# Optimization experiments

Hardware: AMD Instinct MI355X
Metric: run time of the kernel (lower is better)

The kernel has to match this reference:

```python
import jax, jax.numpy as jnp
import numpy as np

SR = 16000
FLOOR = 60.0
EPS = 1e-12

# ---------- numpy helpers replicating the torch control flow (plan building) ----------

def _hann(n):
    # torch.hann_window default periodic=True: 0.5 - 0.5*cos(2*pi*k/n)
    if n <= 0:
        return np.zeros((0,), np.float32)
    return (0.5 - 0.5 * np.cos(2.0 * np.pi * np.arange(n) / n)).astype(np.float32)


def _interp_linear(p, T):
    # torch F.interpolate(mode='linear', align_corners=False) on [1,1,S] -> [1,1,T]
    S = p.shape[0]
    pos = (np.arange(T, dtype=np.float64) + 0.5) * (S / T) - 0.5
    pos = np.clip(pos, 0.0, S - 1)
    lo = np.floor(pos).astype(np.int64)
    hi = np.minimum(lo + 1, S - 1)
    frac = pos - lo
    return (p[lo] * (1.0 - frac) + p[hi] * frac).astype(np.float32)


def _find_voiced(f0, i):
    sub = f0[i:]
    if sub.size == 0:
        return None
    flag = (sub > 0.0).astype(np.int64)
    flag[0] = 0
    if not flag.any():
        return None
    idx = int(flag.argmax())
    rest = flag[idx:]
    z = np.nonzero(rest == 0)[0]
    cnt = int(z[0]) if z.size else int(rest.size)
    left = i + idx
    return left, left + cnt


def _find_allpeaks(sig, f0, sr, floor=FLOOR):
    T = sig.shape[0]
    gpeak = float(np.abs(sig).max())

    def find_peak(i, dir_):
        w = int(sr / max(float(f0[i]), floor))
        s = max(i - w // 2, 0)
        if dir_ == 'left':
            cl, cr = max(int(i - 1.75 * w), 0), max(int(i - 1.3 * w), 0)
        else:
            cl, cr = int(i + 0.3 * w), int(i + 0.75 * w)
        if cl == cr or T - cl < w or s + w > T:
            return w, -1.0, i, 0.0
        seg = np.lib.stride_tricks.sliding_window_view(sig[cl:min(T, cr + w)], w)
        segn = seg / np.maximum(np.linalg.norm(seg, axis=-1, keepdims=True), EPS)
        tmpl = sig[s:s + w]
        tmpl = tmpl / max(float(np.linalg.norm(tmpl)), EPS)
        corr = segn @ tmpl
        r = int(corr.argmax())
        return w, float(corr[r]), i + (r + cl) - s, float(np.abs(seg[r]).max())

    added_right, i, peaks = -1e308, 0, []
    while True:
        v = _find_voiced(f0, i)
        if v is None:
            break
        left, right = v
        middle = (left + right) // 2
        w = int(sr / float(f0[middle]))
        s = max(middle - w // 2, 0)
        win = sig[s:s + w]
        mn, imn = float(win.min()), int(win.argmin())
        mx, imx = float(win.max()), int(win.argmax())
        if mn == mx:
            i = middle
        else:
            i = s + (imn if abs(mn) > abs(mx) else imx)
        backup = i
        while True:
            w, corr, i, peak = find_peak(i, 'left')
            if corr == -1.0:
                i -= w
            if i < left:
                if corr > 0.7 and peak > 0.023333 * gpeak and i - added_right > 0.8 * w:
                    peaks.append(i)
                break
            if corr > 0.3 and (peak == 0.0 or peak > 0.01 * gpeak):
                if i - added_right > 0.8 * w:
                    peaks.append(i)
        i = backup
        while True:
            w, corr, i, peak = find_peak(i, 'right')
            if corr == -1.0:
                i += w
            if i >= right:
                if corr > 0.7 and peak > 0.023333 * gpeak:
                    peaks.append(i)
                    added_right = i
                break
            if corr > 0.3 and (peak == 0.0 or peak > 0.01 * gpeak):
                peaks.append(i)
                added_right = i
        i = right
    if not peaks:
        return None
    return np.clip(np.sort(np.array(peaks, np.int64)), 0, T - 1)


def _psola_plan(T, f0, peaks, sr, floor=FLOOR):
    # Returns (dst_idx, src_idx, wgt, tail_i) s.t.
    #   new = zeros; new[dst] += wgt * x[src]; new[tail_i:] = x[tail_i:]
    max_w = 1.25 * sr / float(f0[f0 > 0].min())
    dsts, srcs, ws = [], [], []

    def add_op(dst0, src0, win):
        n = win.shape[0]
        if n > 0:
            dsts.append(dst0 + np.arange(n, dtype=np.int64))
            srcs.append(src0 + np.arange(n, dtype=np.int64))
            ws.append(win)

    i = 0
    while i < T:
        v = _find_voiced(f0, i)
        if v is None:
            break
        left_v, right_v = v
        add_op(i, i, _hann(left_v - i))  # hann fade over unvoiced gap
        while left_v < right_v:
            p = int(np.abs(peaks - left_v).argmin())
            period = int(sr / max(float(f0[left_v]), floor))
            lw = rw = period // 2
            if p > 0 and peaks[p] - peaks[p - 1] <= max_w:
                lw = min(int(peaks[p] - peaks[p - 1]), lw)
            if p < len(peaks) - 1 and peaks[p + 1] - peaks[p] <= max_w:
                rw = min(int(peaks[p + 1] - peaks[p]), rw)
            li = max(int(peaks[p]) - lw, 0)
            ri = int(peaks[p]) + rw
            ival = (ri - li) // 2
            if ival <= 0:  # safety guard vs duplicate peaks (torch code would stall)
                left_v += max(period, 1)
                continue
            win = _hann(2 * ival)
            a, b = left_v - ival, left_v + ival
            st, sp, _ = slice(a, b).indices(T)        # python/torch slice semantics
            dst_len = max(0, sp - st)
            src_len = max(0, min(T, li + 2 * ival) - li)
            seglen = min(dst_len, src_len)
            st2, _, _ = slice(a, a + seglen).indices(T)
            add_op(st2, li, win[:seglen])
            left_v += ival * 2
        i = right_v
    if dsts:
        dst = np.concatenate(dsts)
        src = np.concatenate(srcs)
        wgt = np.concatenate(ws)
    else:
        dst = np.zeros((0,), np.int64)
        src = np.zeros((0,), np.int64)
        wgt = np.zeros((0,), np.float32)
    return dst, src, wgt, min(i, T)


def build_plan(snd_np, pitch_np, pitch_shift, pitch_range):
    T = snd_np.shape[0]
    x = snd_np - snd_np.mean()
    f0 = _interp_linear(pitch_np, T)
    peaks = _find_allpeaks(x, f0, SR)
    assert peaks is not None, 'no peaks found'
    voiced = np.sort(f0[f0 > 0.0])
    median = float(voiced[(voiced.size - 1) // 2]) * pitch_shift  # torch median = lower middle
    f0 = f0 * pitch_shift
    f0 = np.where(f0 > 0.0, median + (f0 - median) * pitch_range, 0.0)
    return _psola_plan(T, f0, peaks, SR)


# ---------- harness entry points ----------

def setup_inputs() -> dict:
    key = jax.random.key(0)
    k1, k2 = jax.random.split(key)
    T = 3_840_000   # 240 s at 16 kHz
    S = 15_000      # pitch frames (hop 256)
    t = jnp.arange(T, dtype=jnp.float32) / SR
    # pitched signal + noise so peak correlation thresholds fire like real speech
    snd = 0.5 * jnp.sin(2.0 * jnp.pi * 130.0 * t) + 0.05 * jax.random.normal(k1, (T,), jnp.float32)
    base = 100.0 + 80.0 * jax.random.uniform(k2, (S,), jnp.float32)
    voiced = ((jnp.arange(S) // 250) % 5) != 4   # voiced runs with unvoiced gaps
    pitch = jnp.where(voiced, base, 0.0)
    return {'snd': snd, 'pitch': pitch, 'pitch_shift': 1.2, 'pitch_range': 0.8}


def reference(snd, pitch, pitch_shift, pitch_range):
    snd_np = np.asarray(snd, np.float32)
    pitch_np = np.asarray(pitch, np.float32)
    dst, src, wgt, tail = build_plan(snd_np, pitch_np, float(pitch_shift), float(pitch_range))
    dst_j = jnp.asarray(dst)
    src_j = jnp.asarray(src)
    wgt_j = jnp.asarray(wgt)
    x = snd - jnp.mean(snd)
    out = jnp.zeros_like(x).at[dst_j].add(wgt_j * x[src_j])
    # final unvoiced tail is a SET (overwrites any OLA spill), matching torch order
    mask = jnp.arange(x.shape[0]) >= tail
    return jnp.where(mask, x, out)
```

## Files before the change

kernel.cpp:

```cpp
#include <hip/hip_runtime.h>
#include <math.h>
#include <limits.h>

typedef long long ll;

#define MAXCHAIN 4096
#define MAXP 49152
#define MAXOPS 49152
#define MAXR 64
#define PART_OFF 4096
#define CHAINS_OFF 16384
#define PEAKS_OFF (CHAINS_OFF + 128 * MAXCHAIN * 4)
#define OPS_OFF (PEAKS_OFF + MAXP * 4)
#define F0_OFF (OPS_OFF + (size_t)MAXOPS * 16)

static __device__ const double TWOPI = 6.283185307179586;

struct Ctrl {
  double gpeak, max_w, ps64;
  long long k_rem, tail;
  float mean32, median_raw, md32, minv_scaled32;
  unsigned amax_bits, minf0_bits, prefix;
  int cnt_pos, shift, n_starts, n_ends, nregions, n_peaks, n_ops, slab;
  int hist[256];
  int region_start[MAXR], region_end[MAXR];
  int chain_cnt[128];
  int chain_off[129];
  int region_ops[MAXR];
};

__device__ __forceinline__ double dmul(double a, double b) { return __dmul_rn(a, b); }
__device__ __forceinline__ double dadd(double a, double b) { return __dadd_rn(a, b); }
__device__ __forceinline__ double dsub(double a, double b) { return __dadd_rn(a, -b); }
__device__ __forceinline__ float fmul(float a, float b) { return __fmul_rn(a, b); }
__device__ __forceinline__ float fadd(float a, float b) { return __fadd_rn(a, b); }
__device__ __forceinline__ float fsub(float a, float b) { return __fadd_rn(a, -b); }

__device__ __forceinline__ float xval(const float* snd, float mean, ll t) {
  return fsub(snd[t], mean);
}

__device__ __forceinline__ float div_exact(float x, float d, float r) {
  float q = __fmul_rn(x, r);
  float e = __fmaf_rn(-d, q, x);
  return __fmaf_rn(e, r, q);
}

__device__ float f0_at(const float* pitch, ll t, ll S, double ratio) {
  double pos = dsub(dmul(dadd((double)t, 0.5), ratio), 0.5);
  double hi = (double)(S - 1);
  pos = fmin(fmax(pos, 0.0), hi);
  double fl = floor(pos);
  ll lo = (ll)fl;
  if (lo < 0) lo = 0;
  if (lo > S - 1) lo = S - 1;
  ll hii = lo + 1; if (hii > S - 1) hii = S - 1;
  double frac = dsub(pos, fl);
  double om = dsub(1.0, frac);
  double v = dadd(dmul((double)pitch[lo], om), dmul((double)pitch[hii], frac));
  return (float)v;
}

__device__ __forceinline__ ll frame_lo(ll t, ll S, double ratio) {
  double pos = dsub(dmul(dadd((double)t, 0.5), ratio), 0.5);
  pos = fmin(fmax(pos, 0.0), (double)(S - 1));
  ll lo = (ll)floor(pos);
  if (lo < 0) lo = 0;
  if (lo > S - 1) lo = S - 1;
  return lo;
}

__device__ __forceinline__ float f0_lds(const float* __restrict__ lpitch, int p0, int p1,
                                        const float* __restrict__ pitch,
                                        ll t, ll S, double ratio) {
  double pos = dsub(dmul(dadd((double)t, 0.5), ratio), 0.5);
  pos = fmin(fmax(pos, 0.0), (double)(S - 1));
  double fl = floor(pos);
  ll lo = (ll)fl;
  if (lo < 0) lo = 0;
  if (lo > S - 1) lo = S - 1;
  ll hii = lo + 1; if (hii > S - 1) hii = S - 1;
  double frac = dsub(pos, fl);
  double om = dsub(1.0, frac);
  float plo = (lo >= p0 && lo <= p1) ? lpitch[(int)(lo - p0)] : pitch[lo];
  float phi = (hii >= p0 && hii <= p1) ? lpitch[(int)(hii - p0)] : pitch[hii];
  return (float)dadd(dmul((double)plo, om), dmul((double)phi, frac));
}

__device__ void pw2_blk(const float* __restrict__ buf, int bA, int bB, int n,
                        float& outA, float& outB, float& pkB) {
  if (n < 8) {
    float ra = 0.f;
    for (int i = 0; i < n; ++i) { float x = buf[bA + i]; ra = fadd(ra, fmul(x, x)); }
    float rb = 0.f;
    for (int i = 0; i < n; ++i) {
      float x = buf[bB + i];
      pkB = fmaxf(pkB, fabsf(x));
      rb = fadd(rb, fmul(x, x));
    }
    outA = ra; outB = rb; return;
  }
  float ca[8], cb[8], na[8], nb[8], rA[8], rB[8];
  #pragma unroll
  for (int j = 0; j < 8; ++j) ca[j] = buf[bA + j];
  #pragma unroll
  for (int j = 0; j < 8; ++j) cb[j] = buf[bB + j];
  int lim = n - (n & 7);
  bool hn = (8 < lim);
  if (hn) {
    #pragma unroll
    for (int j = 0; j < 8; ++j) na[j] = buf[bA + 8 + j];
    #pragma unroll
    for (int j = 0; j < 8; ++j) nb[j] = buf[bB + 8 + j];
  }
  #pragma unroll
  for (int j = 0; j < 8; ++j) pkB = fmaxf(pkB, fabsf(cb[j]));
  #pragma unroll
  for (int j = 0; j < 8; ++j) rA[j] = fmul(ca[j], ca[j]);
  #pragma unroll
  for (int j = 0; j < 8; ++j) rB[j] = fmul(cb[j], cb[j]);
  for (int i = 8; i < lim; i += 8) {
    #pragma unroll
    for (int j = 0; j < 8; ++j) { ca[j] = na[j]; cb[j] = nb[j]; }
    bool hn2 = (i + 8 < lim);
    if (hn2) {
      #pragma unroll
      for (int j = 0; j < 8; ++j) na[j] = buf[bA + i + 8 + j];
      #pragma unroll
      for (int j = 0; j < 8; ++j) nb[j] = buf[bB + i + 8 + j];
    }
    #pragma unroll
    for (int j = 0; j < 8; ++j) {
      pkB = fmaxf(pkB, fabsf(cb[j]));
      rA[j] = fadd(rA[j], fmul(ca[j], ca[j]));
      rB[j] = fadd(rB[j], fmul(cb[j], cb[j]));
    }
  }
  float resA = fadd(fadd(fadd(rA[0], rA[1]), fadd(rA[2], rA[3])),
                    fadd(fadd(rA[4], rA[5]), fadd(rA[6], rA[7])));
  float resB = fadd(fadd(fadd(rB[0], rB[1]), fadd(rB[2], rB[3])),
                    fadd(fadd(rB[4], rB[5]), fadd(rB[6], rB[7])));
  for (int i = lim; i < n; ++i) {
    float xa = buf[bA + i];
    resA = fadd(resA, fmul(xa, xa));
    float xb = buf[bB + i];
    pkB = fmaxf(pkB, fabsf(xb));
    resB = fadd(resB, fmul(xb, xb));
  }
  outA = resA; outB = resB;
}

__device__ void pw2_sq(const float* __restrict__ buf, int bA, int bB, int n,
                       float& oA, float& oB, float& pkB) {
  if (n <= 128) { pw2_blk(buf, bA, bB, n, oA, oB, pkB); return; }
  int n2 = (n >> 1); n2 -= (n2 & 7);
  float a1, b1;
  pw2_blk(buf, bA, bB, n2, a1, b1, pkB);
  int m = n - n2;
  if (m <= 128) {
    float a2, b2;
    pw2_blk(buf, bA + n2, bB + n2, m, a2, b2, pkB);
    oA = fadd(a1, a2); oB = fadd(b1, b2);
  } else {
    int m2 = (m >> 1); m2 -= (m2 & 7);
    float a2a, b2a, a2b, b2b;
    pw2_blk(buf, bA + n2, bB + n2, m2, a2a, b2a, pkB);
    pw2_blk(buf, bA + n2 + m2, bB + n2 + m2, m - m2, a2b, b2b, pkB);
    oA = fadd(a1, fadd(a2a, a2b)); oB = fadd(b1, fadd(b2a, b2b));
  }
}

__device__ float pw1_blk(const float* __restrict__ buf, int base, int n, float& pk) {
  if (n < 8) {
    float res = 0.0f;
    for (int i = 0; i < n; ++i) {
      float x = buf[base + i];
      pk = fmaxf(pk, fabsf(x));
      res = fadd(res, fmul(x, x));
    }
    return res;
  }
  float cb[8], nb[8], rB[8];
  #pragma unroll
  for (int j = 0; j < 8; ++j) cb[j] = buf[base + j];
  int lim = n - (n & 7);
  bool hn = (8 < lim);
  if (hn) {
    #pragma unroll
    for (int j = 0; j < 8; ++j) nb[j] = buf[base + 8 + j];
  }
  #pragma unroll
  for (int j = 0; j < 8; ++j) pk = fmaxf(pk, fabsf(cb[j]));
  #pragma unroll
  for (int j = 0; j < 8; ++j) rB[j] = fmul(cb[j], cb[j]);
  for (int i = 8; i < lim; i += 8) {
    #pragma unroll
    for (int j = 0; j < 8; ++j) cb[j] = nb[j];
    bool hn2 = (i + 8 < lim);
    if (hn2) {
      #pragma unroll
      for (int j = 0; j < 8; ++j) nb[j] = buf[base + i + 8 + j];
    }
    #pragma unroll
    for (int j = 0; j < 8; ++j) {
      pk = fmaxf(pk, fabsf(cb[j]));
      rB[j] = fadd(rB[j], fmul(cb[j], cb[j]));
    }
  }
  float res = fadd(fadd(fadd(rB[0], rB[1]), fadd(rB[2], rB[3])),
                   fadd(fadd(rB[4], rB[5]), fadd(rB[6], rB[7])));
  for (int i = lim; i < n; ++i) {
    float y = buf[base + i];
    pk = fmaxf(pk, fabsf(y));
    res = fadd(res, fmul(y, y));
  }
  return res;
}

__device__ float pw1_sq(const float* __restrict__ buf, int base, int n, float& pk) {
  if (n <= 128) return pw1_blk(buf, base, n, pk);
  int n2 = (n >> 1); n2 -= (n2 & 7);
  float a = pw1_blk(buf, base, n2, pk);
  int m = n - n2;
  float b;
  if (m <= 128) {
    b = pw1_blk(buf, base + n2, m, pk);
  } else {
    int m2 = (m >> 1); m2 -= (m2 & 7);
    float b1 = pw1_blk(buf, base + n2, m2, pk);
    float b2 = pw1_blk(buf, base + n2 + m2, m - m2, pk);
    b = fadd(b1, b2);
  }
  return fadd(a, b);
}

__device__ float dot_lds(const float* __restrict__ buf, int base, float d, float r,
                         const float* __restrict__ tm, int w) {
  float acc[8];
  #pragma unroll
  for (int j = 0; j < 8; ++j) acc[j] = 0.f;
  int lim = w - (w & 7);
  if (lim > 0) {
    float cs[8], ct[8], ns[8], nt[8];
    #pragma unroll
    for (int j = 0; j < 8; ++j) cs[j] = buf[base + j];
    #pragma unroll
    for (int j = 0; j < 8; ++j) ct[j] = tm[j];
    for (int k = 0; k < lim; k += 8) {
      bool hn = (k + 8 < lim);
      if (hn) {
        #pragma unroll
        for (int j = 0; j < 8; ++j) ns[j] = buf[base + k + 8 + j];
        #pragma unroll
        for (int j = 0; j < 8; ++j) nt[j] = tm[k + 8 + j];
      }
      #pragma unroll
      for (int j = 0; j < 8; ++j)
        acc[j] = __fmaf_rn(div_exact(cs[j], d, r), ct[j], acc[j]);
      if (hn) {
        #pragma unroll
        for (int j = 0; j < 8; ++j) { cs[j] = ns[j]; ct[j] = nt[j]; }
      }
    }
  }
  #pragma unroll
  for (int j = 0; j < 7; ++j)
    if (lim + j < w)
      acc[j] = __fmaf_rn(div_exact(buf[base + lim + j], d, r), tm[lim + j], acc[j]);
  return fadd(fadd(fadd(acc[0], acc[1]), fadd(acc[2], acc[3])),
              fadd(fadd(acc[4], acc[5]), fadd(acc[6], acc[7])));
}

__global__ void k_init(char* wsb) {
  Ctrl* c = (Ctrl*)wsb;
  int t = threadIdx.x;
  for (int b = t; b < 256; b += blockDim.x) c->hist[b] = 0;
  for (int b = t; b < 128; b += blockDim.x) c->chain_cnt[b] = 0;
  for (int b = t; b < MAXR; b += blockDim.x) c->region_ops[b] = 0;
  if (t == 0) {
    c->amax_bits = 0u; c->minf0_bits = 0xFFFFFFFFu;
    c->cnt_pos = 0; c->n_starts = 0; c->n_ends = 0; c->n_ops = 0;
    c->nregions = 0; c->n_peaks = 0; c->tail = 0; c->slab = MAXOPS;
  }
}

__global__ void k_sum_partial(const float* __restrict__ snd, ll T, char* wsb) {
  __shared__ double sd[256];
  double local = 0.0;
  ll stride = (ll)gridDim.x * blockDim.x;
  for (ll t = (ll)blockIdx.x * blockDim.x + threadIdx.x; t < T; t += stride)
    local += (double)snd[t];
  sd[threadIdx.x] = local; __syncthreads();
  for (int o = 128; o > 0; o >>= 1) {
    if ((int)threadIdx.x < o) sd[threadIdx.x] += sd[threadIdx.x + o];
    __syncthreads();
  }
  if (threadIdx.x == 0) ((double*)(wsb + PART_OFF))[blockIdx.x] = sd[0];
}

__global__ void k_sum_final(char* wsb, ll T, int nparts) {
  __shared__ double sd[256];
  double local = 0.0;
  const double* p = (const double*)(wsb + PART_OFF);
  for (int i = threadIdx.x; i < nparts; i += blockDim.x) local += p[i];
  sd[threadIdx.x] = local; __syncthreads();
  for (int o = 128; o > 0; o >>= 1) {
    if ((int)threadIdx.x < o) sd[threadIdx.x] += sd[threadIdx.x + o];
    __syncthreads();
  }
  if (threadIdx.x == 0) ((Ctrl*)wsb)->mean32 = (float)(sd[0] / (double)T);
}

__global__ void k_f0(const float* __restrict__ pitch, ll T, ll S, double ratio,
                     unsigned* __restrict__ bits) {
  ll stride = (ll)gridDim.x * blockDim.x;
  for (ll t = (ll)blockIdx.x * blockDim.x + threadIdx.x; t < T; t += stride)
    bits[t] = __float_as_uint(f0_at(pitch, t, S, ratio));
}

__global__ void k_scan(const float* __restrict__ snd, const float* __restrict__ pitch,
                       ll T, ll S, double ratio, char* wsb,
                       const unsigned* __restrict__ f0bits, int cached) {
  Ctrl* c = (Ctrl*)wsb;
  float mean = c->mean32;
  __shared__ unsigned smax[256]; __shared__ unsigned smin[256]; __shared__ int scnt[256];
  unsigned mymax = 0u, mymin = 0xFFFFFFFFu; int mycnt = 0;
  ll stride = (ll)gridDim.x * blockDim.x;
  for (ll t = (ll)blockIdx.x * blockDim.x + threadIdx.x; t < T; t += stride) {
    float xv = xval(snd, mean, t);
    unsigned ab = __float_as_uint(fabsf(xv));
    if (ab > mymax) mymax = ab;
    float f = cached ? __uint_as_float(f0bits[t]) : f0_at(pitch, t, S, ratio);
    bool pos = (f > 0.0f);
    if (pos) { ++mycnt; unsigned fb = __float_as_uint(f); if (fb < mymin) mymin = fb; }
    if (t >= 1) {
      float fp = cached ? __uint_as_float(f0bits[t - 1]) : f0_at(pitch, t - 1, S, ratio);
      bool posp = (fp > 0.0f);
      if (pos && (t == 1 || !posp)) {
        int id = atomicAdd(&c->n_starts, 1);
        if (id < MAXR) c->region_start[id] = (int)t;
      }
      if (!pos && posp && (t - 1) >= 1) {
        int id = atomicAdd(&c->n_ends, 1);
        if (id < MAXR) c->region_end[id] = (int)t;
      }
    }
    if (t == T - 1 && pos) {
      int id = atomicAdd(&c->n_ends, 1);
      if (id < MAXR) c->region_end[id] = (int)T;
    }
  }
  smax[threadIdx.x] = mymax; smin[threadIdx.x] = mymin; scnt[threadIdx.x] = mycnt;
  __syncthreads();
  for (int o = 128; o > 0; o >>= 1) {
    if ((int)threadIdx.x < o) {
      if (smax[threadIdx.x + o] > smax[threadIdx.x]) smax[threadIdx.x] = smax[threadIdx.x + o];
      if (smin[threadIdx.x + o] < smin[threadIdx.x]) smin[threadIdx.x] = smin[threadIdx.x + o];
      scnt[threadIdx.x] += scnt[threadIdx.x + o];
    }
    __syncthreads();
  }
  if (threadIdx.x == 0) {
    atomicMax(&c->amax_bits, smax[0]);
    atomicMin(&c->minf0_bits, smin[0]);
    atomicAdd(&c->cnt_pos, scnt[0]);
  }
}

__global__ void k_prep(char* wsb, const float* ps) {
  Ctrl* c = (Ctrl*)wsb;
  int ns = c->n_starts; if (ns > MAXR) ns = MAXR;
  int ne = c->n_ends; if (ne > MAXR) ne = MAXR;
  for (int a = 1; a < ns; ++a) {
    int v = c->region_start[a]; int b = a - 1;
    while (b >= 0 && c->region_start[b] > v) { c->region_start[b + 1] = c->region_start[b]; --b; }
    c->region_start[b + 1] = v;
  }
  for (int a = 1; a < ne; ++a) {
    int v = c->region_end[a]; int b = a - 1;
    while (b >= 0 && c->region_end[b] > v) { c->region_end[b + 1] = c->region_end[b]; --b; }
    c->region_end[b + 1] = v;
  }
  int nr = ns < ne ? ns : ne;
  c->nregions = nr;
  c->tail = (nr > 0) ? (ll)c->region_end[nr - 1] : 0;
  c->gpeak = (double)__uint_as_float(c->amax_bits);
  ll cnt = (ll)c->cnt_pos; if (cnt < 1) cnt = 1;
  c->k_rem = (cnt - 1) / 2;
  c->prefix = 0u; c->shift = 24;
  c->slab = MAXOPS / (nr > 0 ? nr : 1);
  double p64 = (double)ps[0];
  c->ps64 = round(p64 * 1e7) / 1e7;
}

__global__ void k_hist(const float* __restrict__ pitch, ll T, ll S, double ratio, char* wsb,
                       const unsigned* __restrict__ f0bits, int cached) {
  Ctrl* c = (Ctrl*)wsb;
  __shared__ int h[256];
  for (int b = threadIdx.x; b < 256; b += blockDim.x) h[b] = 0;
  __syncthreads();
  int shift = c->shift;
  unsigned pref = c->prefix;
  unsigned himask = (shift == 24) ? 0u : ((~0u) << (shift + 8));
  ll stride = (ll)gridDim.x * blockDim.x;
  for (ll t = (ll)blockIdx.x * blockDim.x + threadIdx.x; t < T; t += stride) {
    float f; unsigned bits;
    if (cached) { bits = f0bits[t]; f = __uint_as_float(bits); }
    else { f = f0_at(pitch, t, S, ratio); bits = __float_as_uint(f); }
    if (f > 0.0f) {
      if ((bits & himask) == (pref & himask)) atomicAdd(&h[(bits >> shift) & 255], 1);
    }
  }
  __syncthreads();
  for (int b = threadIdx.x; b < 256; b += blockDim.x) if (h[b]) atomicAdd(&c->hist[b], h[b]);
}

__global__ void k_sel(char* wsb, const float* ps, const float* pr) {
  Ctrl* c = (Ctrl*)wsb;
  int shift = c->shift;
  ll k = c->k_rem;
  ll run = 0; int pick = 255;
  for (int b = 0; b < 256; ++b) {
    ll h = (ll)c->hist[b];
    if (run + h > k) { pick = b; break; }
    run += h;
  }
  c->prefix |= ((unsigned)pick) << shift;
  c->k_rem = k - run;
  for (int b = 0; b < 256; ++b) c->hist[b] = 0;
  if (shift == 0) {
    float mraw = __uint_as_float(c->prefix);
    c->median_raw = mraw;
    double md = dmul((double)mraw, c->ps64);
    float md32 = (float)md;
    c->md32 = md32;
    float minf = __uint_as_float(c->minf0_bits);
    float u = fmul(minf, ps[0]);
    float sc = fadd(md32, fmul(fsub(u, md32), pr[0]));
    c->minv_scaled32 = sc;
    c->max_w = 20000.0 / (double)sc;
  }
  c->shift = shift - 8;
}

#define WALK_MAXI 400000
#define WPS 1664

__global__ __launch_bounds__(64) void k_walks(const float* __restrict__ snd,
                                              const float* __restrict__ pitch,
                                              ll T, ll S, double ratio, char* wsb) {
  Ctrl* c = (Ctrl*)wsb;
  int chain = blockIdx.x;
  int reg = chain >> 1, dir = chain & 1;
  if (reg >= c->nregions) return;
  int* mybuf = ((int*)(wsb + CHAINS_OFF)) + (ll)chain * MAXCHAIN;
  ll left = (ll)c->region_start[reg];
  ll right = (ll)c->region_end[reg];
  float mean = c->mean32;
  double gpeak = c->gpeak;
  int lane = threadIdx.x;

  __shared__ float lx[640];
  __shared__ float ltm[272];
  __shared__ float lpitch[WPS];

  ll tA = left - 600; if (tA < 0) tA = 0;
  ll tB = right + 600; if (tB > T - 1) tB = T - 1;
  ll p0l = frame_lo(tA, S, ratio);
  ll p1l = frame_lo(tB, S, ratio) + 1; if (p1l > S - 1) p1l = S - 1;
  int p0 = (int)p0l, p1 = (int)p1l;
  int span = p1 - p0 + 1;
  bool puse = (span <= WPS);
  if (puse) {
    for (int k = lane; k < span; k += 64) lpitch[k] = pitch[p0 + k];
  } else { p0 = 0; p1 = -1; }
  __syncthreads();

  ll i;
  {
    ll middle = (left + right) / 2;
    float f0m = f0_lds(lpitch, p0, p1, pitch, middle, S, ratio);
    int w0 = (int)(16000.0 / (double)f0m);
    ll s0 = middle - (ll)(w0 / 2); if (s0 < 0) s0 = 0;
    ll len = T - s0; if (len > (ll)w0) len = (ll)w0;
    float mn = 0.f, mx = 0.f; ll imn = 0, imx = 0; bool first = true;
    for (ll k = 0; k < len; ++k) {
      float v = xval(snd, mean, s0 + k);
      if (first) { mn = mx = v; imn = imx = 0; first = false; }
      else {
        if (v < mn) { mn = v; imn = k; }
        if (v > mx) { mx = v; imx = k; }
      }
    }
    if (mn == mx) i = middle;
    else i = s0 + ((fabs((double)mn) > fabs((double)mx)) ? imn : imx);
  }

  double added_right = -1e308;
  int cnt = 0;
  bool stop = false;

  for (int iter = 0; iter < WALK_MAXI && !stop; ++iter) {
    float f0v = f0_lds(lpitch, p0, p1, pitch, i, S, ratio);
    int w = (int)(16000.0 / fmax((double)f0v, 60.0));
    ll cl, cr;
    if (dir == 0) {
      cl = (ll)dsub((double)i, dmul(1.75, (double)w)); if (cl < 0) cl = 0;
      cr = (ll)dsub((double)i, dmul(1.3, (double)w)); if (cr < 0) cr = 0;
    } else {
      cl = (ll)dadd((double)i, dmul(0.3, (double)w));
      cr = (ll)dadd((double)i, dmul(0.75, (double)w));
    }
    ll s = i - (ll)(w / 2); if (s < 0) s = 0;
    bool valid = !(cl == cr || (T - cl) < (ll)w || (s + (ll)w) > T);
    double corrd; ll ipos; double peakd;
    if (!valid) { corrd = -1.0; ipos = i; peakd = 0.0; }
    else {
      ll L = cr + (ll)w; if (L > T) L = T; L -= cl;
      int ncand = (int)(L - (ll)w + 1);
      ll lo = (s < cl) ? s : cl;
      ll hiA = s + (ll)w;
      ll hiB = cl + L;
      ll hi = (hiA > hiB) ? hiA : hiB;
      int len = (int)(hi - lo);
      float stg[10];
      #pragma unroll
      for (int j = 0; j < 10; ++j) {
        ll a = lo + (ll)(j * 64) + lane;
        if (a > T - 1) a = T - 1;
        stg[j] = snd[a];
      }
      __syncthreads();
      #pragma unroll
      for (int j = 0; j < 10; ++j) {
        int k = j * 64 + lane;
        if (k < len) lx[k] = fsub(stg[j], mean);
      }
      __syncthreads();
      int toff = (int)(s - lo);
      int coff = (int)(cl - lo);
      int r0 = lane;
      int rc0 = (r0 < ncand) ? r0 : (ncand - 1);
      float pk0 = 0.0f;
      float tsq, csq0;
      pw2_sq(lx, toff, coff + rc0, w, tsq, csq0, pk0);
      float tn = __fsqrt_rn(tsq);
      float tdiv = (float)fmax((double)tn, 1e-12);
      float rt = __fdiv_rn(1.0f, tdiv);
      float nr0 = __fsqrt_rn(csq0);
      float divr0 = fmaxf(nr0, (float)1e-12);
      float rr0 = __fdiv_rn(1.0f, divr0);
      float pk1 = 0.0f, divr1 = 1.0f, rr1 = 1.0f;
      int rc1 = 0;
      bool has1 = (ncand > 64);
      if (has1) {
        int r1 = lane + 64;
        rc1 = (r1 < ncand) ? r1 : (ncand - 1);
        float nr1 = __fsqrt_rn(pw1_sq(lx, coff + rc1, w, pk1));
        divr1 = fmaxf(nr1, (float)1e-12);
        rr1 = __fdiv_rn(1.0f, divr1);
      }
      for (int k = lane; k < w; k += 64) ltm[k] = div_exact(lx[toff + k], tdiv, rt);
      __syncthreads();
      float co0 = dot_lds(lx, coff + rc0, divr0, rr0, ltm, w);
      float co1 = -INFINITY;
      if (has1) {
        co1 = dot_lds(lx, coff + rc1, divr1, rr1, ltm, w);
        if (lane + 64 >= ncand) co1 = -INFINITY;
      }
      float bv = (r0 < ncand) ? co0 : -INFINITY;
      int bi = (r0 < ncand) ? r0 : 0x7FFFFFFF;
      {
        int i1 = lane + 64;
        if (co1 > bv || (co1 == bv && i1 < bi)) { bv = co1; bi = i1; }
      }
      for (int off = 32; off > 0; off >>= 1) {
        float ov = __shfl_xor(bv, off);
        int oi = __shfl_xor(bi, off);
        if (ov > bv || (ov == bv && oi < bi)) { bv = ov; bi = oi; }
      }
      corrd = (double)bv;
      ipos = i + ((ll)bi + cl) - s;
      {
        int ol = bi & 63;
        float p0f = __shfl(pk0, ol);
        float p1f = __shfl(pk1, ol);
        peakd = (double)((bi < 64) ? p0f : p1f);
      }
    }
    ll inew;
    if (dir == 0) {
      inew = (corrd == -1.0) ? (i - (ll)w) : ipos;
      if (inew < left) {
        if (corrd > 0.7 && peakd > dmul(0.023333, gpeak) &&
            (dsub((double)inew, added_right) > dmul(0.8, (double)w))) {
          if (cnt < MAXCHAIN) { if (lane == 0) mybuf[cnt] = (int)inew; ++cnt; }
        }
        stop = true;
      } else {
        if (corrd > 0.3 && (peakd == 0.0 || peakd > dmul(0.01, gpeak))) {
          if (dsub((double)inew, added_right) > dmul(0.8, (double)w)) {
            if (cnt < MAXCHAIN) { if (lane == 0) mybuf[cnt] = (int)inew; ++cnt; }
          }
        }
        i = inew;
      }
    } else {
      inew = (corrd == -1.0) ? (i + (ll)w) : ipos;
      if (inew >= right) {
        if (corrd > 0.7 && peakd > dmul(0.023333, gpeak)) {
          if (cnt < MAXCHAIN) { if (lane == 0) mybuf[cnt] = (int)inew; ++cnt; }
        }
        stop = true;
      } else {
        if (corrd > 0.3 && (peakd == 0.0 || peakd > dmul(0.01, gpeak))) {
          if (cnt < MAXCHAIN) { if (lane == 0) mybuf[cnt] = (int)inew; ++cnt; }
          added_right = (double)inew;
        }
        i = inew;
      }
    }
  }
  if (lane == 0) c->chain_cnt[chain] = cnt;
}

__global__ void k_offsets(char* wsb) {
  Ctrl* c = (Ctrl*)wsb;
  int off = 0;
  for (int ch = 0; ch < 128; ++ch) {
    c->chain_off[ch] = off;
    off += c->chain_cnt[ch];
  }
  c->chain_off[128] = off;
  c->n_peaks = (off > MAXP) ? MAXP : off;
}

__global__ void k_gather(char* wsb, ll T) {
  Ctrl* c = (Ctrl*)wsb;
  int chain = blockIdx.x;
  int cnt = c->chain_cnt[chain];
  int off = c->chain_off[chain];
  const int* mybuf = ((const int*)(wsb + CHAINS_OFF)) + (ll)chain * MAXCHAIN;
  int* peaks = (int*)(wsb + PEAKS_OFF);
  int dir = chain & 1;
  for (int k = threadIdx.x; k < cnt; k += blockDim.x) {
    if (off + k < MAXP) {
      int v = dir ? mybuf[k] : mybuf[cnt - 1 - k];
      if (v < 0) v = 0;
      if ((ll)v > T - 1) v = (int)(T - 1);
      peaks[off + k] = v;
    }
  }
}

#define PSLDS 3584
#define PPS 2048

__global__ __launch_bounds__(64) void k_psola(const float* __restrict__ pitch, ll T, ll S,
                                              double ratio, char* wsb,
                                              const float* ps, const float* pr) {
  Ctrl* c = (Ctrl*)wsb;
  int r = blockIdx.x;
  if (r >= c->nregions) return;
  const int* peaks = (const int*)(wsb + PEAKS_OFF);
  int np = c->n_peaks;
  int tid = threadIdx.x;
  ll left = (ll)c->region_start[r], right = (ll)c->region_end[r];

  __shared__ int lp[PSLDS];
  __shared__ float lpitch[PPS];
  __shared__ int sh_g0, sh_g1, sh_use;

  ll tA = left - 600; if (tA < 0) tA = 0;
  ll tB = right + 600; if (tB > T - 1) tB = T - 1;
  ll p0l = frame_lo(tA, S, ratio);
  ll p1l = frame_lo(tB, S, ratio) + 1; if (p1l > S - 1) p1l = S - 1;
  int p0 = (int)p0l, p1 = (int)p1l;
  int span = p1 - p0 + 1;
  if (span <= PPS) {
    for (int k = tid; k < span; k += 64) lpitch[k] = pitch[p0 + k];
  } else { p0 = 0; p1 = -1; }

  if (np > 0) {
    if (tid == 0) {
      int lo = 0, hi = np;
      ll tgt = left - 512;
      while (lo < hi) { int m = (lo + hi) >> 1; if ((ll)peaks[m] < tgt) lo = m + 1; else hi = m; }
      int a = lo;
      lo = 0; hi = np; tgt = right + 512;
      while (lo < hi) { int m = (lo + hi) >> 1; if ((ll)peaks[m] < tgt) lo = m + 1; else hi = m; }
      int b = lo;
      a -= 4; if (a < 0) a = 0;
      b += 4; if (b > np) b = np;
      sh_g0 = a; sh_g1 = b; sh_use = (b - a <= PSLDS) ? 1 : 0;
    }
    __syncthreads();
    if (sh_use) {
      for (int k = sh_g0 + tid; k < sh_g1; k += 64) lp[k - sh_g0] = peaks[k];
    }
  }
  __syncthreads();
  if (tid != 0) return;

  int g0 = (np > 0 && sh_use) ? sh_g0 : 0;
  const int* pk = (np > 0 && sh_use) ? lp : peaks;

  int slab = c->slab;
  int4* myops = ((int4*)(wsb + OPS_OFF)) + (ll)r * slab;
  int cnt = 0;
  ll prev_end = (r == 0) ? 0 : (ll)c->region_end[r - 1];
  ll lv = left, rv = right;
  double max_w = c->max_w;
  float md32 = c->md32, psv = ps[0], prv = pr[0];

  ll gapn = lv - prev_end;
  if (gapn > 0) {
    if (cnt < slab) myops[cnt] = make_int4((int)prev_end, (int)prev_end, (int)gapn, (int)gapn);
    ++cnt;
  }
  if (np > 0) {
    int j;
    {
      int loJ = 0, hiJ = np;
      while (loJ < hiJ) {
        int mid = (loJ + hiJ) >> 1;
        if ((ll)peaks[mid] < lv) loJ = mid + 1; else hiJ = mid;
      }
      j = loJ;
    }
    for (long itc = 0; itc < 2000000 && lv < rv; ++itc) {
      float f = f0_lds(lpitch, p0, p1, pitch, lv, S, ratio);
      float u = fmul(f, psv);
      float fs = (!(u > 0.0f)) ? 0.0f : fadd(md32, fmul(fsub(u, md32), prv));
      int period = (int)(16000.0 / fmax((double)fs, 60.0));
      int lw = period / 2, rw = period / 2;
      while (j < np && (ll)pk[j - g0] < lv) ++j;
      ll dl = (j > 0) ? (lv - (ll)pk[j - 1 - g0]) : LLONG_MAX;
      ll dr = (j < np) ? ((ll)pk[j - g0] - lv) : LLONG_MAX;
      int p;
      if (dl <= dr) {
        int q = j - 1; int v = pk[q - g0];
        while (q > 0 && pk[q - 1 - g0] == v) --q;
        p = q;
      } else {
        int q = j; int v = pk[q - g0];
        while (q > 0 && pk[q - 1 - g0] == v) --q;
        p = q;
      }
      if (p > 0) {
        ll g = (ll)pk[p - g0] - (ll)pk[p - 1 - g0];
        if ((double)g <= max_w && g < (ll)lw) lw = (int)g;
      }
      if (p < np - 1) {
        ll g = (ll)pk[p + 1 - g0] - (ll)pk[p - g0];
        if ((double)g <= max_w && g < (ll)rw) rw = (int)g;
      }
      ll li = (ll)pk[p - g0] - (ll)lw; if (li < 0) li = 0;
      ll ri = (ll)pk[p - g0] + (ll)rw;
      ll ival = (ri - li) / 2;
      if (ival <= 0) { lv += (period > 1 ? (ll)period : 1); continue; }
      ll a = lv - ival, b = lv + ival;
      ll st = (a < 0) ? ((a + T > 0) ? a + T : 0) : ((a < T) ? a : T);
      ll sp = (b < 0) ? ((b + T > 0) ? b + T : 0) : ((b < T) ? b : T);
      ll dst_len = sp - st; if (dst_len < 0) dst_len = 0;
      ll se = li + 2 * ival; if (se > T) se = T;
      ll src_len = se - li; if (src_len < 0) src_len = 0;
      ll seglen = dst_len < src_len ? dst_len : src_len;
      if (seglen > 0) {
        if (cnt < slab) myops[cnt] = make_int4((int)st, (int)li, (int)seglen, (int)(2 * ival));
        ++cnt;
      }
      lv += 2 * ival;
    }
  }
  c->region_ops[r] = (cnt > slab) ? slab : cnt;
}

__global__ void k_scatter(const float* __restrict__ snd, char* wsb, float* out, ll T) {
  Ctrl* c = (Ctrl*)wsb;
  float mean = c->mean32;
  int nr = c->nregions; if (nr > MAXR) nr = MAXR;
  int slab = c->slab;
  const int4* ops = (const int4*)(wsb + OPS_OFF);
  ll total = (ll)nr * slab;
  for (ll idx = blockIdx.x; idx < total; idx += gridDim.x) {
    int r = (int)(idx / slab);
    int o = (int)(idx - (ll)r * slab);
    if (o >= c->region_ops[r]) continue;
    int4 op = ops[(ll)r * slab + o];
    ll dst = (ll)op.x, src = (ll)op.y; int n = op.z, m = op.w;
    for (int k = threadIdx.x; k < n; k += blockDim.x) {
      double ang = dmul(TWOPI, (double)k) / (double)m;
      float w32 = (float)dsub(0.5, dmul(0.5, cos(ang)));
      float val = fmul(w32, xval(snd, mean, src + k));
      atomicAdd(&out[dst + k], val);
    }
  }
}

__global__ void k_final(const float* __restrict__ snd, char* wsb, float* out, ll T) {
  Ctrl* c = (Ctrl*)wsb;
  float mean = c->mean32;
  ll tail = c->tail;
  ll stride = (ll)gridDim.x * blockDim.x;
  for (ll t = (ll)blockIdx.x * blockDim.x + threadIdx.x; t < T; t += stride)
    if (t >= tail) out[t] = xval(snd, mean, t);
}

extern "C" void kernel_launch(void* const* d_in, const int* in_sizes, int n_in,
                              void* d_out, int out_size, void* d_ws, size_t ws_size,
                              hipStream_t stream) {
  ll T = (ll)in_sizes[0];
  ll S = (ll)in_sizes[1];
  const float* snd = (const float*)d_in[0];
  const float* pitch = (const float*)d_in[1];
  const float* ps = (const float*)d_in[2];
  const float* pr = (const float*)d_in[3];
  float* out = (float*)d_out;
  char* wsb = (char*)d_ws;
  double ratio = (double)S / (double)T;

  size_t f0_need = F0_OFF + (size_t)T * 4;
  int cached = (ws_size >= f0_need) ? 1 : 0;
  unsigned* f0bits = (unsigned*)(wsb + F0_OFF);

  k_init<<<1, 256, 0, stream>>>(wsb);
  k_sum_partial<<<1024, 256, 0, stream>>>(snd, T, wsb);
  k_sum_final<<<1, 256, 0, stream>>>(wsb, T, 1024);
  if (cached) k_f0<<<2048, 256, 0, stream>>>(pitch, T, S, ratio, f0bits);
  k_scan<<<2048, 256, 0, stream>>>(snd, pitch, T, S, ratio, wsb, f0bits, cached);
  k_prep<<<1, 1, 0, stream>>>(wsb, ps);
  for (int pass = 0; pass < 4; ++pass) {
    k_hist<<<2048, 256, 0, stream>>>(pitch, T, S, ratio, wsb, f0bits, cached);
    k_sel<<<1, 1, 0, stream>>>(wsb, ps, pr);
  }
  k_walks<<<128, 64, 0, stream>>>(snd, pitch, T, S, ratio, wsb);
  k_offsets<<<1, 1, 0, stream>>>(wsb);
  k_gather<<<128, 64, 0, stream>>>(wsb, T);
  k_psola<<<64, 64, 0, stream>>>(pitch, T, S, ratio, wsb, ps, pr);
  hipMemsetAsync(d_out, 0, (size_t)out_size * sizeof(float), stream);
  k_scatter<<<8192, 128, 0, stream>>>(snd, wsb, out, T);
  k_final<<<2048, 256, 0, stream>>>(snd, wsb, out, T);
}
```

Measured before the change: 11.71 ms.

## Prefetch next walk window, double-buffer LDS, and fuse small launch kernels

```diff
diff --git a/kernel.cpp b/kernel.cpp
--- a/kernel.cpp
+++ b/kernel.cpp
@@ -28,6 +28,12 @@
   int chain_off[129];
   int region_ops[MAXR];
 };
+
+#define WBAR() do { \
+  asm volatile("s_waitcnt lgkmcnt(0)" ::: "memory"); \
+  __builtin_amdgcn_s_barrier(); \
+  __builtin_amdgcn_sched_barrier(0); \
+} while (0)
 
 __device__ __forceinline__ double dmul(double a, double b) { return __dmul_rn(a, b); }
 __device__ __forceinline__ double dadd(double a, double b) { return __dadd_rn(a, b); }
@@ -271,20 +277,19 @@
               fadd(fadd(acc[4], acc[5]), fadd(acc[6], acc[7])));
 }
 
-__global__ void k_init(char* wsb) {
-  Ctrl* c = (Ctrl*)wsb;
-  int t = threadIdx.x;
-  for (int b = t; b < 256; b += blockDim.x) c->hist[b] = 0;
-  for (int b = t; b < 128; b += blockDim.x) c->chain_cnt[b] = 0;
-  for (int b = t; b < MAXR; b += blockDim.x) c->region_ops[b] = 0;
-  if (t == 0) {
-    c->amax_bits = 0u; c->minf0_bits = 0xFFFFFFFFu;
-    c->cnt_pos = 0; c->n_starts = 0; c->n_ends = 0; c->n_ops = 0;
-    c->nregions = 0; c->n_peaks = 0; c->tail = 0; c->slab = MAXOPS;
-  }
-}
-
-__global__ void k_sum_partial(const float* __restrict__ snd, ll T, char* wsb) {
+__global__ void k_init_sum(const float* __restrict__ snd, ll T, char* wsb) {
+  Ctrl* c = (Ctrl*)wsb;
+  if (blockIdx.x == 0) {
+    int t = threadIdx.x;
+    for (int b = t; b < 256; b += blockDim.x) c->hist[b] = 0;
+    for (int b = t; b < 128; b += blockDim.x) c->chain_cnt[b] = 0;
+    for (int b = t; b < MAXR; b += blockDim.x) c->region_ops[b] = 0;
+    if (t == 0) {
+      c->amax_bits = 0u; c->minf0_bits = 0xFFFFFFFFu;
+      c->cnt_pos = 0; c->n_starts = 0; c->n_ends = 0; c->n_ops = 0;
+      c->nregions = 0; c->n_peaks = 0; c->tail = 0; c->slab = MAXOPS;
+    }
+  }
   __shared__ double sd[256];
   double local = 0.0;
   ll stride = (ll)gridDim.x * blockDim.x;
@@ -311,16 +316,9 @@
   if (threadIdx.x == 0) ((Ctrl*)wsb)->mean32 = (float)(sd[0] / (double)T);
 }
 
-__global__ void k_f0(const float* __restrict__ pitch, ll T, ll S, double ratio,
-                     unsigned* __restrict__ bits) {
-  ll stride = (ll)gridDim.x * blockDim.x;
-  for (ll t = (ll)blockIdx.x * blockDim.x + threadIdx.x; t < T; t += stride)
-    bits[t] = __float_as_uint(f0_at(pitch, t, S, ratio));
-}
-
 __global__ void k_scan(const float* __restrict__ snd, const float* __restrict__ pitch,
                        ll T, ll S, double ratio, char* wsb,
-                       const unsigned* __restrict__ f0bits, int cached) {
+                       unsigned* __restrict__ f0bits, int cached) {
   Ctrl* c = (Ctrl*)wsb;
   float mean = c->mean32;
   __shared__ unsigned smax[256]; __shared__ unsigned smin[256]; __shared__ int scnt[256];
@@ -330,11 +328,12 @@
     float xv = xval(snd, mean, t);
     unsigned ab = __float_as_uint(fabsf(xv));
     if (ab > mymax) mymax = ab;
-    float f = cached ? __uint_as_float(f0bits[t]) : f0_at(pitch, t, S, ratio);
+    float f = f0_at(pitch, t, S, ratio);
+    if (cached) f0bits[t] = __float_as_uint(f);
     bool pos = (f > 0.0f);
     if (pos) { ++mycnt; unsigned fb = __float_as_uint(f); if (fb < mymin) mymin = fb; }
     if (t >= 1) {
-      float fp = cached ? __uint_as_float(f0bits[t - 1]) : f0_at(pitch, t - 1, S, ratio);
+      float fp = f0_at(pitch, t - 1, S, ratio);
       bool posp = (fp > 0.0f);
       if (pos && (t == 1 || !posp)) {
         int id = atomicAdd(&c->n_starts, 1);
@@ -445,6 +444,8 @@
 
 #define WALK_MAXI 400000
 #define WPS 1664
+#define PFN 8
+#define PFW (PFN * 64)
 
 __global__ __launch_bounds__(64) void k_walks(const float* __restrict__ snd,
                                               const float* __restrict__ pitch,
@@ -460,7 +461,8 @@
   double gpeak = c->gpeak;
   int lane = threadIdx.x;
 
-  __shared__ float lx[640];
+  __shared__ float lxA[640];
+  __shared__ float lxB[640];
   __shared__ float ltm[272];
   __shared__ float lpitch[WPS];
 
@@ -499,6 +501,10 @@
   double added_right = -1e308;
   int cnt = 0;
   bool stop = false;
+  int bsel = 0;
+  float pstg[PFN];
+  ll pf_base = 0;
+  bool pf_ok = false;
 
   for (int iter = 0; iter < WALK_MAXI && !stop; ++iter) {
     float f0v = f0_lds(lpitch, p0, p1, pitch, i, S, ratio);
@@ -514,8 +520,17 @@
     ll s = i - (ll)(w / 2); if (s < 0) s = 0;
     bool valid = !(cl == cr || (T - cl) < (ll)w || (s + (ll)w) > T);
     double corrd; ll ipos; double peakd;
-    if (!valid) { corrd = -1.0; ipos = i; peakd = 0.0; }
-    else {
+    if (!valid) {
+      corrd = -1.0; ipos = i; peakd = 0.0;
+      ll pb = dir ? (i + (ll)(w >> 2) - 8) : (i - 3 * (ll)w - 16);
+      bool ok = (pb >= 0) && (pb + PFW <= T);
+      if (ok) {
+        #pragma unroll
+        for (int j = 0; j < PFN; ++j) pstg[j] = snd[pb + (ll)(j * 64) + lane];
+        pf_base = pb;
+      }
+      pf_ok = ok;
+    } else {
       ll L = cr + (ll)w; if (L > T) L = T; L -= cl;
       int ncand = (int)(L - (ll)w + 1);
       ll lo = (s < cl) ? s : cl;
@@ -523,27 +538,62 @@
       ll hiB = cl + L;
       ll hi = (hiA > hiB) ? hiA : hiB;
       int len = (int)(hi - lo);
-      float stg[10];
-      #pragma unroll
-      for (int j = 0; j < 10; ++j) {
-        ll a = lo + (ll)(j * 64) + lane;
-        if (a > T - 1) a = T - 1;
-        stg[j] = snd[a];
-      }
-      __syncthreads();
-      #pragma unroll
-      for (int j = 0; j < 10; ++j) {
-        int k = j * 64 + lane;
-        if (k < len) lx[k] = fsub(stg[j], mean);
-      }
-      __syncthreads();
+      float* lxb = bsel ? lxB : lxA;
+      bool covered = pf_ok && (lo >= pf_base) && (hi <= pf_base + PFW);
+      if (covered) {
+        #pragma unroll
+        for (int j = 0; j < PFN; ++j) {
+          int k = (int)((pf_base + (ll)(j * 64) + lane) - lo);
+          if (k >= 0 && k < len) lxb[k] = fsub(pstg[j], mean);
+        }
+      } else {
+        float stg[10];
+        #pragma unroll
+        for (int j = 0; j < 5; ++j) {
+          ll a = lo + (ll)(j * 64) + lane;
+          if (a > T - 1) a = T - 1;
+          stg[j] = snd[a];
+        }
+        bool big = (len > 320);
+        if (big) {
+          #pragma unroll
+          for (int j = 5; j < 10; ++j) {
+            ll a = lo + (ll)(j * 64) + lane;
+            if (a > T - 1) a = T - 1;
+            stg[j] = snd[a];
+          }
+        }
+        #pragma unroll
+        for (int j = 0; j < 5; ++j) {
+          int k = j * 64 + lane;
+          if (k < len) lxb[k] = fsub(stg[j], mean);
+        }
+        if (big) {
+          #pragma unroll
+          for (int j = 5; j < 10; ++j) {
+            int k = j * 64 + lane;
+            if (k < len) lxb[k] = fsub(stg[j], mean);
+          }
+        }
+      }
+      {
+        ll pb = dir ? (i + (ll)(w >> 2) - 8) : (i - 3 * (ll)w - 16);
+        bool ok = (pb >= 0) && (pb + PFW <= T);
+        if (ok) {
+          #pragma unroll
+          for (int j = 0; j < PFN; ++j) pstg[j] = snd[pb + (ll)(j * 64) + lane];
+          pf_base = pb;
+        }
+        pf_ok = ok;
+      }
+      WBAR();
       int toff = (int)(s - lo);
       int coff = (int)(cl - lo);
       int r0 = lane;
       int rc0 = (r0 < ncand) ? r0 : (ncand - 1);
       float pk0 = 0.0f;
       float tsq, csq0;
-      pw2_sq(lx, toff, coff + rc0, w, tsq, csq0, pk0);
+      pw2_sq(lxb, toff, coff + rc0, w, tsq, csq0, pk0);
       float tn = __fsqrt_rn(tsq);
       float tdiv = (float)fmax((double)tn, 1e-12);
       float rt = __fdiv_rn(1.0f, tdiv);
@@ -556,16 +606,16 @@
       if (has1) {
         int r1 = lane + 64;
         rc1 = (r1 < ncand) ? r1 : (ncand - 1);
-        float nr1 = __fsqrt_rn(pw1_sq(lx, coff + rc1, w, pk1));
+        float nr1 = __fsqrt_rn(pw1_sq(lxb, coff + rc1, w, pk1));
         divr1 = fmaxf(nr1, (float)1e-12);
         rr1 = __fdiv_rn(1.0f, divr1);
       }
-      for (int k = lane; k < w; k += 64) ltm[k] = div_exact(lx[toff + k], tdiv, rt);
-      __syncthreads();
-      float co0 = dot_lds(lx, coff + rc0, divr0, rr0, ltm, w);
+      for (int k = lane; k < w; k += 64) ltm[k] = div_exact(lxb[toff + k], tdiv, rt);
+      WBAR();
+      float co0 = dot_lds(lxb, coff + rc0, divr0, rr0, ltm, w);
       float co1 = -INFINITY;
       if (has1) {
-        co1 = dot_lds(lx, coff + rc1, divr1, rr1, ltm, w);
+        co1 = dot_lds(lxb, coff + rc1, divr1, rr1, ltm, w);
         if (lane + 64 >= ncand) co1 = -INFINITY;
       }
       float bv = (r0 < ncand) ? co0 : -INFINITY;
@@ -587,6 +637,7 @@
         float p1f = __shfl(pk1, ol);
         peakd = (double)((bi < 64) ? p0f : p1f);
       }
+      bsel ^= 1;
     }
     ll inew;
     if (dir == 0) {
@@ -624,22 +675,12 @@
   if (lane == 0) c->chain_cnt[chain] = cnt;
 }
 
-__global__ void k_offsets(char* wsb) {
-  Ctrl* c = (Ctrl*)wsb;
-  int off = 0;
-  for (int ch = 0; ch < 128; ++ch) {
-    c->chain_off[ch] = off;
-    off += c->chain_cnt[ch];
-  }
-  c->chain_off[128] = off;
-  c->n_peaks = (off > MAXP) ? MAXP : off;
-}
-
 __global__ void k_gather(char* wsb, ll T) {
   Ctrl* c = (Ctrl*)wsb;
   int chain = blockIdx.x;
   int cnt = c->chain_cnt[chain];
-  int off = c->chain_off[chain];
+  int off = 0;
+  for (int ch = 0; ch < chain; ++ch) off += c->chain_cnt[ch];
   const int* mybuf = ((const int*)(wsb + CHAINS_OFF)) + (ll)chain * MAXCHAIN;
   int* peaks = (int*)(wsb + PEAKS_OFF);
   int dir = chain & 1;
@@ -650,6 +691,11 @@
       if ((ll)v > T - 1) v = (int)(T - 1);
       peaks[off + k] = v;
     }
+  }
+  if (chain == 0 && threadIdx.x == 0) {
+    int tot = 0;
+    for (int ch = 0; ch < 128; ++ch) tot += c->chain_cnt[ch];
+    c->n_peaks = (tot > MAXP) ? MAXP : tot;
   }
 }
 
@@ -824,10 +870,8 @@
   int cached = (ws_size >= f0_need) ? 1 : 0;
   unsigned* f0bits = (unsigned*)(wsb + F0_OFF);
 
-  k_init<<<1, 256, 0, stream>>>(wsb);
-  k_sum_partial<<<1024, 256, 0, stream>>>(snd, T, wsb);
+  k_init_sum<<<1024, 256, 0, stream>>>(snd, T, wsb);
   k_sum_final<<<1, 256, 0, stream>>>(wsb, T, 1024);
-  if (cached) k_f0<<<2048, 256, 0, stream>>>(pitch, T, S, ratio, f0bits);
   k_scan<<<2048, 256, 0, stream>>>(snd, pitch, T, S, ratio, wsb, f0bits, cached);
   k_prep<<<1, 1, 0, stream>>>(wsb, ps);
   for (int pass = 0; pass < 4; ++pass) {
@@ -835,7 +879,6 @@
     k_sel<<<1, 1, 0, stream>>>(wsb, ps, pr);
   }
   k_walks<<<128, 64, 0, stream>>>(snd, pitch, T, S, ratio, wsb);
-  k_offsets<<<1, 1, 0, stream>>>(wsb);
   k_gather<<<128, 64, 0, stream>>>(wsb, T);
   k_psola<<<64, 64, 0, stream>>>(pitch, T, S, ratio, wsb, ps, pr);
   hipMemsetAsync(d_out, 0, (size_t)out_size * sizeof(float), stream);
```

Measured after the change: 11.63 ms. No clear change (-0.7%).
